# Kernel tuning notes

Hardware: AMD Instinct MI355X
Metric: run time of the kernel (lower is better)

The kernel has to match this reference:

```python
import jax, jax.numpy as jnp
import numpy as np
import math

L, H, P = 16384, 128, 256


def setup_inputs() -> dict:
    key = jax.random.key(0)
    k = jax.random.split(key, 6)
    return {
        "input_sequence": jax.random.normal(k[0], (L, H), dtype=jnp.float32),
        "A_diag": jax.random.uniform(k[1], (P,), dtype=jnp.float32),
        "B": (jax.random.uniform(k[2], (P, H, 2), dtype=jnp.float32) * 2.0 - 1.0) / math.sqrt(H),
        "C": (jax.random.uniform(k[3], (H, P, 2), dtype=jnp.float32) * 2.0 - 1.0) / math.sqrt(P),
        "D": jax.random.normal(k[4], (H,), dtype=jnp.float32),
        "steps": jax.random.uniform(k[5], (P,), dtype=jnp.float32),
    }


def _binop(qi, qj):
    # 2x2 block-diagonal matrix product + affine state propagation, per channel.
    iA, iB, iC, iD, ib1, ib2 = qi
    jA, jB, jC, jD, jb1, jb2 = qj
    return (
        jA * iA + jB * iC,
        jA * iB + jB * iD,
        jC * iA + jD * iC,
        jC * iB + jD * iD,
        jA * ib1 + jB * ib2 + jb1,
        jC * ib1 + jD * ib2 + jb2,
    )


def reference(input_sequence, A_diag, B, C, D, steps):
    # LinOSS-IM discretization (implicit)
    A = jax.nn.relu(A_diag)                      # (P,)
    dt = jax.nn.sigmoid(steps)                   # (P,)
    Bc = B[..., 0] + 1j * B[..., 1]              # (P,H) complex64
    Cc = C[..., 0] + 1j * C[..., 1]              # (H,P) complex64

    Bu = input_sequence @ Bc.T                   # (L,P) complex64

    schur = 1.0 / (1.0 + dt ** 2 * A)
    M11 = 1.0 - dt ** 2 * A * schur
    M12 = -dt * A * schur
    M21 = dt * schur
    M22 = schur

    ones = jnp.ones((input_sequence.shape[0], A.shape[0]), dtype=input_sequence.dtype)
    F1 = M11 * Bu * dt                           # (L,P) complex
    F2 = M21 * Bu * dt

    elems = (M11 * ones, M12 * ones, M21 * ones, M22 * ones, F1, F2)
    _, _, _, _, _, x2 = jax.lax.associative_scan(_binop, elems)  # scan over L

    ys = jnp.real(x2 @ Cc.T)                     # (L,H)
    return ys + input_sequence * D
```

## Files before the change

kernel.cpp:

```cpp
#include <hip/hip_runtime.h>
#include <math.h>

#define L 16384
#define H 128
#define P 256
#define CL 32
#define NCH (L/CL)
#define GS 16
#define NG (NCH/GS)
#define FW 8
#define KDIM 512
#define NBU 512
#define NFLAGS (NCH*FW + NG*FW + 1)

typedef __attribute__((ext_vector_type(8))) short short8;
typedef __attribute__((ext_vector_type(4))) float f32x4;

__device__ inline unsigned short f2bf(float f){
  union { float f; unsigned u; } v; v.f = f;
  unsigned u = v.u;
  u += 0x7fffu + ((u >> 16) & 1u);
  return (unsigned short)(u >> 16);
}
__device__ inline float bf2f(unsigned short s){
  union { unsigned u; float f; } v; v.u = ((unsigned)s) << 16;
  return v.f;
}

struct Params { float M11,M12,M21,M22,s1,s2; };

__device__ inline Params get_params(const float* A_diag, const float* steps, int p){
  float A = A_diag[p]; A = A > 0.f ? A : 0.f;
  float dt = 1.f/(1.f + expf(-steps[p]));
  float schur = 1.f/(1.f + dt*dt*A);
  Params q;
  q.M11 = 1.f - dt*dt*A*schur;
  q.M12 = -dt*A*schur;
  q.M21 = dt*schur;
  q.M22 = schur;
  q.s1 = q.M11*dt;
  q.s2 = q.M21*dt;
  return q;
}

__device__ inline unsigned long long aload(const unsigned long long* p){
  return __hip_atomic_load((unsigned long long*)p, __ATOMIC_RELAXED,
                           __HIP_MEMORY_SCOPE_AGENT);
}
__device__ inline void apub(unsigned long long* p, unsigned long long v){
  (void)__hip_atomic_exchange(p, v, __ATOMIC_RELAXED, __HIP_MEMORY_SCOPE_AGENT);
}
__device__ inline void fpub(unsigned* p){
  (void)__hip_atomic_exchange(p, 1u, __ATOMIC_RELAXED, __HIP_MEMORY_SCOPE_AGENT);
}
__device__ inline void wait_flag(unsigned* f){
  while (__hip_atomic_load(f, __ATOMIC_RELAXED, __HIP_MEMORY_SCOPE_AGENT) == 0u)
    __builtin_amdgcn_s_sleep(1);
}

__global__ __launch_bounds__(512) void prep_w(const float* __restrict__ B,
                                              const float* __restrict__ Cw,
                                              unsigned short* __restrict__ BWswz,
                                              unsigned short* __restrict__ Bswz,
                                              unsigned* __restrict__ flags){
  int gidx = blockIdx.x*512 + threadIdx.x;
  if (gidx < NFLAGS) flags[gidx] = 0u;
  if (gidx < H*NBU){
    int k = gidx >> 9, n = gidx & 511;
    int p = n & 255, c2 = n >> 8;
    float v = B[((size_t)p*H + k)*2 + c2];
    BWswz[((size_t)(k>>3)*NBU + n)*8 + (k&7)] = f2bf(v);
  } else {
    int g2 = gidx - H*NBU;
    int k = g2 >> 7, n = g2 & 127;
    float v = (k < P) ? Cw[((size_t)n*P + k)*2]
                      : -Cw[((size_t)n*P + (k-P))*2 + 1];
    Bswz[((size_t)(k>>3)*H + n)*8 + (k&7)] = f2bf(v);
  }
}

__global__ __launch_bounds__(512, 2) void linoss_fused(
    const float* __restrict__ in,
    const float* __restrict__ A_diag,
    const float* __restrict__ steps,
    const float* __restrict__ Dv,
    const unsigned short* __restrict__ BWswz,
    const unsigned short* __restrict__ Bswz,
    unsigned long long* __restrict__ finals,
    unsigned long long* __restrict__ gfin,
    unsigned* __restrict__ flag1,
    unsigned* __restrict__ flag2,
    unsigned* __restrict__ counter,
    float* __restrict__ out)
{
  __shared__ unsigned short sX[CL][NBU+8];
  __shared__ int s_cid;
  const int tid = threadIdx.x;
  if (tid == 0)
    s_cid = (int)__hip_atomic_fetch_add(counter, 1u, __ATOMIC_RELAXED,
                                        __HIP_MEMORY_SCOPE_AGENT);
  __syncthreads();
  const int c = s_cid;

  {
    int lane = tid & 63, w = tid >> 6;
    int ml = lane & 15, quad = lane >> 4;
    int mt = w & 1, ng = w >> 1;
    int lm0 = mt*16;
    const float* aptr = in + (size_t)(c*CL + lm0 + ml)*H + quad*8;
    float4 fa[8];
    #pragma unroll
    for (int ks=0; ks<4; ks++){
      fa[2*ks]   = *(const float4*)(aptr + ks*32);
      fa[2*ks+1] = *(const float4*)(aptr + ks*32 + 4);
    }
    short8 av[4];
    #pragma unroll
    for (int ks=0; ks<4; ks++){
      union { short8 s; unsigned short u[8]; } o;
      o.u[0]=f2bf(fa[2*ks].x); o.u[1]=f2bf(fa[2*ks].y);
      o.u[2]=f2bf(fa[2*ks].z); o.u[3]=f2bf(fa[2*ks].w);
      o.u[4]=f2bf(fa[2*ks+1].x); o.u[5]=f2bf(fa[2*ks+1].y);
      o.u[6]=f2bf(fa[2*ks+1].z); o.u[7]=f2bf(fa[2*ks+1].w);
      av[ks] = o.s;
    }
    f32x4 acc[8];
    #pragma unroll
    for (int t=0;t<8;t++) acc[t] = (f32x4){0.f,0.f,0.f,0.f};
    #pragma unroll
    for (int ks=0; ks<4; ks++){
      short8 bv[8];
      #pragma unroll
      for (int t=0;t<8;t++)
        bv[t] = *(const short8*)(BWswz + ((size_t)(ks*4+quad)*NBU + (ng*8+t)*16 + ml)*8);
      #pragma unroll
      for (int t=0;t<8;t++)
        acc[t] = __builtin_amdgcn_mfma_f32_16x16x32_bf16(av[ks], bv[t], acc[t], 0, 0, 0);
    }
    #pragma unroll
    for (int t=0;t<8;t++){
      int n = (ng*8+t)*16 + ml;
      #pragma unroll
      for (int r=0;r<4;r++)
        sX[lm0 + quad*4 + r][n] = f2bf(acc[t][r]);
    }
  }
  __syncthreads();

  const int p = tid & 255, part = tid >> 8;
  Params q = get_params(A_diag, steps, p);
  float Ta=q.M11, Tb=q.M12, Tc=q.M21, Td=q.M22;
  #pragma unroll
  for (int s=0;s<5;s++){
    float na=Ta*Ta+Tb*Tc, nb=Ta*Tb+Tb*Td, nc=Tc*Ta+Td*Tc, nd=Tc*Tb+Td*Td;
    Ta=na;Tb=nb;Tc=nc;Td=nd;
  }
  float fx1=0.f, fx2=0.f;
  {
    float u[CL];
    #pragma unroll
    for (int i=0;i<CL;i++) u[i] = bf2f(sX[i][part*256 + p]);
    #pragma unroll
    for (int i=0;i<CL;i++){
      float n1 = q.M11*fx1 + q.M12*fx2 + q.s1*u[i];
      float n2 = q.M21*fx1 + q.M22*fx2 + q.s2*u[i];
      fx1 = n1; fx2 = n2;
    }
  }
  {
    union { unsigned long long u; float2 f; } w; w.f = make_float2(fx1,fx2);
    apub(&finals[(size_t)(part*NCH + c)*P + p], w.u);
  }
  asm volatile("s_waitcnt vmcnt(0)" ::: "memory");
  if ((tid & 63) == 0) fpub(&flag1[c*FW + (tid >> 6)]);

  const int g = c >> 4, iw = c & (GS-1);
  const unsigned long long* Fp = finals + (size_t)part*NCH*P + (size_t)g*GS*P + p;

  float sa=1.f, sb=0.f, sc=0.f, sd=1.f;
  {
    float wa=Ta, wb=Tb, wc=Tc, wd=Td;
    #pragma unroll
    for (int bit=0; bit<4; bit++){
      if ((iw>>bit)&1){
        float na = wa*sa + wb*sc, nb = wa*sb + wb*sd;
        float nc = wc*sa + wd*sc, nd = wc*sb + wd*sd;
        sa=na; sb=nb; sc=nc; sd=nd;
      }
      float qa = wa*wa + wb*wc, qb = wa*wb + wb*wd;
      float qc = wc*wa + wd*wc, qd = wc*wb + wd*wd;
      wa=qa; wb=qb; wc=qc; wd=qd;
    }
  }
  float ga=Ta, gb=Tb, gc=Tc, gd=Td;
  #pragma unroll
  for (int s=0;s<4;s++){
    float na=ga*ga+gb*gc, nb=ga*gb+gb*gd, nc=gc*ga+gd*gc, nd=gc*gb+gd*gd;
    ga=na;gb=nb;gc=nc;gd=nd;
  }

  float z1=0.f, z2v=0.f;
  {
    if (tid < iw*FW) wait_flag(&flag1[(g*GS + (tid>>3))*FW + (tid&7)]);
    __syncthreads();
    unsigned long long v[GS-1];
    #pragma unroll
    for (int j=0;j<GS-1;j++)
      if (j < iw) v[j] = aload(Fp + (size_t)j*P);
    #pragma unroll
    for (int j=0;j<GS-1;j++){
      if (j < iw){
        union { unsigned long long u; float2 f; } w; w.u = v[j];
        float n1 = Ta*z1 + Tb*z2v + w.f.x;
        float n2 = Tc*z1 + Td*z2v + w.f.y;
        z1=n1; z2v=n2;
      }
    }
  }

  if (iw == GS-1){
    float t1 = Ta*z1 + Tb*z2v + fx1;
    float t2 = Tc*z1 + Td*z2v + fx2;
    union { unsigned long long u; float2 f; } w; w.f = make_float2(t1,t2);
    apub(&gfin[(size_t)(part*NG + g)*P + p], w.u);
    asm volatile("s_waitcnt vmcnt(0)" ::: "memory");
    if ((tid & 63) == 0) fpub(&flag2[g*FW + (tid >> 6)]);
  }

  if (tid < g*FW) wait_flag(&flag2[tid]);
  __syncthreads();

  {
    float y1=0.f, y2=0.f;
    {
      const unsigned long long* Gp = gfin + (size_t)part*NG*P + p;
      #pragma unroll
      for (int half=0; half<2; half++){
        unsigned long long v[16];
        #pragma unroll
        for (int j=0;j<16;j++){
          int jj = half*16+j;
          if (jj < g) v[j] = aload(Gp + (size_t)jj*P);
        }
        #pragma unroll
        for (int j=0;j<16;j++){
          int jj = half*16+j;
          if (jj < g){
            union { unsigned long long u; float2 f; } w; w.u = v[j];
            float n1 = ga*y1 + gb*y2 + w.f.x;
            float n2 = gc*y1 + gd*y2 + w.f.y;
            y1=n1; y2=n2;
          }
        }
      }
    }
    float x1 = sa*y1 + sb*y2 + z1;
    float x2 = sc*y1 + sd*y2 + z2v;
    float u[CL];
    #pragma unroll
    for (int i=0;i<CL;i++) u[i] = bf2f(sX[i][part*256 + p]);
    unsigned short hw[CL];
    #pragma unroll
    for (int i=0;i<CL;i++){
      float n1 = q.M11*x1 + q.M12*x2 + q.s1*u[i];
      float n2 = q.M21*x1 + q.M22*x2 + q.s2*u[i];
      x1 = n1; x2 = n2;
      hw[i] = f2bf(x2);
    }
    #pragma unroll
    for (int i=0;i<CL;i++) sX[i][part*256 + p] = hw[i];
  }
  __syncthreads();

  {
    int lane = tid & 63, w = tid >> 6;
    int ml = lane & 15, quad = lane >> 4;
    int mt = w & 1;
    int ntb = (w >> 1) * 2;
    f32x4 acc[2];
    acc[0] = (f32x4){0.f,0.f,0.f,0.f};
    acc[1] = (f32x4){0.f,0.f,0.f,0.f};
    for (int ks=0; ks<KDIM/32; ks++){
      short8 av = *(const short8*)&sX[mt*16 + ml][ks*32 + quad*8];
      short8 bv0 = *(const short8*)(Bswz + ((size_t)(ks*4+quad)*H + (ntb+0)*16 + ml)*8);
      short8 bv1 = *(const short8*)(Bswz + ((size_t)(ks*4+quad)*H + (ntb+1)*16 + ml)*8);
      acc[0] = __builtin_amdgcn_mfma_f32_16x16x32_bf16(av, bv0, acc[0], 0, 0, 0);
      acc[1] = __builtin_amdgcn_mfma_f32_16x16x32_bf16(av, bv1, acc[1], 0, 0, 0);
    }
    #pragma unroll
    for (int j=0;j<2;j++){
      int h = (ntb+j)*16 + ml;
      float dv = Dv[h];
      #pragma unroll
      for (int r=0;r<4;r++){
        int l = c*CL + mt*16 + quad*4 + r;
        out[(size_t)l*H + h] = acc[j][r] + in[(size_t)l*H + h]*dv;
      }
    }
  }
}

extern "C" void kernel_launch(void* const* d_in, const int* in_sizes, int n_in,
                              void* d_out, int out_size, void* d_ws, size_t ws_size,
                              hipStream_t stream) {
  const float* in     = (const float*)d_in[0];
  const float* A_diag = (const float*)d_in[1];
  const float* B      = (const float*)d_in[2];
  const float* Cw     = (const float*)d_in[3];
  const float* Dv     = (const float*)d_in[4];
  const float* steps  = (const float*)d_in[5];
  float* out = (float*)d_out;

  unsigned short* BWswz = (unsigned short*)d_ws;
  unsigned short* Bswz  = BWswz + (size_t)H*NBU;
  unsigned long long* finals = (unsigned long long*)(Bswz + (size_t)KDIM*H);
  unsigned long long* gfin   = finals + (size_t)2*NCH*P;
  unsigned* flags = (unsigned*)(gfin + (size_t)2*NG*P);
  unsigned* flag1 = flags;
  unsigned* flag2 = flags + NCH*FW;
  unsigned* counter = flags + NCH*FW + NG*FW;

  prep_w<<<256, 512, 0, stream>>>(B, Cw, BWswz, Bswz, flags);
  linoss_fused<<<NCH, 512, 0, stream>>>(in, A_diag, steps, Dv, BWswz, Bswz,
                                        finals, gfin, flag1, flag2, counter, out);
}
```

Baseline: 104.6 us.

## Double block size to 1024 threads and split MFMA work across more waves

Result: slower. 115.4 us (+10.3%).

```diff
diff --git a/kernel.cpp b/kernel.cpp
--- a/kernel.cpp
+++ b/kernel.cpp
@@ -79,7 +79,7 @@
   }
 }
 
-__global__ __launch_bounds__(512, 2) void linoss_fused(
+__global__ __launch_bounds__(1024, 4) void linoss_fused(
     const float* __restrict__ in,
     const float* __restrict__ A_diag,
     const float* __restrict__ steps,
@@ -108,38 +108,32 @@
     int mt = w & 1, ng = w >> 1;
     int lm0 = mt*16;
     const float* aptr = in + (size_t)(c*CL + lm0 + ml)*H + quad*8;
-    float4 fa[8];
+    short8 av[4];
     #pragma unroll
     for (int ks=0; ks<4; ks++){
-      fa[2*ks]   = *(const float4*)(aptr + ks*32);
-      fa[2*ks+1] = *(const float4*)(aptr + ks*32 + 4);
-    }
-    short8 av[4];
+      float4 f0 = *(const float4*)(aptr + ks*32);
+      float4 f1 = *(const float4*)(aptr + ks*32 + 4);
+      union { short8 s; unsigned short u[8]; } o;
+      o.u[0]=f2bf(f0.x); o.u[1]=f2bf(f0.y); o.u[2]=f2bf(f0.z); o.u[3]=f2bf(f0.w);
+      o.u[4]=f2bf(f1.x); o.u[5]=f2bf(f1.y); o.u[6]=f2bf(f1.z); o.u[7]=f2bf(f1.w);
+      av[ks] = o.s;
+    }
+    f32x4 acc[4];
+    #pragma unroll
+    for (int t=0;t<4;t++) acc[t] = (f32x4){0.f,0.f,0.f,0.f};
     #pragma unroll
     for (int ks=0; ks<4; ks++){
-      union { short8 s; unsigned short u[8]; } o;
-      o.u[0]=f2bf(fa[2*ks].x); o.u[1]=f2bf(fa[2*ks].y);
-      o.u[2]=f2bf(fa[2*ks].z); o.u[3]=f2bf(fa[2*ks].w);
-      o.u[4]=f2bf(fa[2*ks+1].x); o.u[5]=f2bf(fa[2*ks+1].y);
-      o.u[6]=f2bf(fa[2*ks+1].z); o.u[7]=f2bf(fa[2*ks+1].w);
-      av[ks] = o.s;
-    }
-    f32x4 acc[8];
-    #pragma unroll
-    for (int t=0;t<8;t++) acc[t] = (f32x4){0.f,0.f,0.f,0.f};
-    #pragma unroll
-    for (int ks=0; ks<4; ks++){
-      short8 bv[8];
-      #pragma unroll
-      for (int t=0;t<8;t++)
-        bv[t] = *(const short8*)(BWswz + ((size_t)(ks*4+quad)*NBU + (ng*8+t)*16 + ml)*8);
-      #pragma unroll
-      for (int t=0;t<8;t++)
+      short8 bv[4];
+      #pragma unroll
+      for (int t=0;t<4;t++)
+        bv[t] = *(const short8*)(BWswz + ((size_t)(ks*4+quad)*NBU + (ng*4+t)*16 + ml)*8);
+      #pragma unroll
+      for (int t=0;t<4;t++)
         acc[t] = __builtin_amdgcn_mfma_f32_16x16x32_bf16(av[ks], bv[t], acc[t], 0, 0, 0);
     }
     #pragma unroll
-    for (int t=0;t<8;t++){
-      int n = (ng*8+t)*16 + ml;
+    for (int t=0;t<4;t++){
+      int n = (ng*4+t)*16 + ml;
       #pragma unroll
       for (int r=0;r<4;r++)
         sX[lm0 + quad*4 + r][n] = f2bf(acc[t][r]);
@@ -147,7 +141,8 @@
   }
   __syncthreads();
 
-  const int p = tid & 255, part = tid >> 8;
+  const int p = tid & 255, part = (tid >> 8) & 1;
+  const bool scanner = (tid < 512);
   Params q = get_params(A_diag, steps, p);
   float Ta=q.M11, Tb=q.M12, Tc=q.M21, Td=q.M22;
   #pragma unroll
@@ -156,23 +151,24 @@
     Ta=na;Tb=nb;Tc=nc;Td=nd;
   }
   float fx1=0.f, fx2=0.f;
-  {
-    float u[CL];
-    #pragma unroll
-    for (int i=0;i<CL;i++) u[i] = bf2f(sX[i][part*256 + p]);
-    #pragma unroll
-    for (int i=0;i<CL;i++){
-      float n1 = q.M11*fx1 + q.M12*fx2 + q.s1*u[i];
-      float n2 = q.M21*fx1 + q.M22*fx2 + q.s2*u[i];
-      fx1 = n1; fx2 = n2;
-    }
-  }
-  {
+  if (scanner){
+    #pragma unroll
+    for (int t0=0; t0<CL; t0+=8){
+      float u[8];
+      #pragma unroll
+      for (int j=0;j<8;j++) u[j] = bf2f(sX[t0+j][part*256 + p]);
+      #pragma unroll
+      for (int j=0;j<8;j++){
+        float n1 = q.M11*fx1 + q.M12*fx2 + q.s1*u[j];
+        float n2 = q.M21*fx1 + q.M22*fx2 + q.s2*u[j];
+        fx1 = n1; fx2 = n2;
+      }
+    }
     union { unsigned long long u; float2 f; } w; w.f = make_float2(fx1,fx2);
     apub(&finals[(size_t)(part*NCH + c)*P + p], w.u);
   }
   asm volatile("s_waitcnt vmcnt(0)" ::: "memory");
-  if ((tid & 63) == 0) fpub(&flag1[c*FW + (tid >> 6)]);
+  if (scanner && (tid & 63) == 0) fpub(&flag1[c*FW + (tid >> 6)]);
 
   const int g = c >> 4, iw = c & (GS-1);
   const unsigned long long* Fp = finals + (size_t)part*NCH*P + (size_t)g*GS*P + p;
@@ -199,53 +195,53 @@
     ga=na;gb=nb;gc=nc;gd=nd;
   }
 
+  if (tid < iw*FW) wait_flag(&flag1[(g*GS + (tid>>3))*FW + (tid&7)]);
+  __syncthreads();
   float z1=0.f, z2v=0.f;
-  {
-    if (tid < iw*FW) wait_flag(&flag1[(g*GS + (tid>>3))*FW + (tid&7)]);
-    __syncthreads();
-    unsigned long long v[GS-1];
-    #pragma unroll
-    for (int j=0;j<GS-1;j++)
-      if (j < iw) v[j] = aload(Fp + (size_t)j*P);
-    #pragma unroll
-    for (int j=0;j<GS-1;j++){
-      if (j < iw){
-        union { unsigned long long u; float2 f; } w; w.u = v[j];
-        float n1 = Ta*z1 + Tb*z2v + w.f.x;
-        float n2 = Tc*z1 + Td*z2v + w.f.y;
-        z1=n1; z2v=n2;
+  if (scanner){
+    for (int t0=0; t0<iw; t0+=8){
+      unsigned long long v[8];
+      #pragma unroll
+      for (int j=0;j<8;j++)
+        if (t0+j < iw) v[j] = aload(Fp + (size_t)(t0+j)*P);
+      #pragma unroll
+      for (int j=0;j<8;j++){
+        if (t0+j < iw){
+          union { unsigned long long u; float2 f; } w; w.u = v[j];
+          float n1 = Ta*z1 + Tb*z2v + w.f.x;
+          float n2 = Tc*z1 + Td*z2v + w.f.y;
+          z1=n1; z2v=n2;
+        }
       }
     }
   }
 
   if (iw == GS-1){
-    float t1 = Ta*z1 + Tb*z2v + fx1;
-    float t2 = Tc*z1 + Td*z2v + fx2;
-    union { unsigned long long u; float2 f; } w; w.f = make_float2(t1,t2);
-    apub(&gfin[(size_t)(part*NG + g)*P + p], w.u);
+    if (scanner){
+      float t1 = Ta*z1 + Tb*z2v + fx1;
+      float t2 = Tc*z1 + Td*z2v + fx2;
+      union { unsigned long long u; float2 f; } w; w.f = make_float2(t1,t2);
+      apub(&gfin[(size_t)(part*NG + g)*P + p], w.u);
+    }
     asm volatile("s_waitcnt vmcnt(0)" ::: "memory");
-    if ((tid & 63) == 0) fpub(&flag2[g*FW + (tid >> 6)]);
+    if (scanner && (tid & 63) == 0) fpub(&flag2[g*FW + (tid >> 6)]);
   }
 
   if (tid < g*FW) wait_flag(&flag2[tid]);
   __syncthreads();
 
-  {
+  if (scanner){
     float y1=0.f, y2=0.f;
     {
       const unsigned long long* Gp = gfin + (size_t)part*NG*P + p;
-      #pragma unroll
-      for (int half=0; half<2; half++){
-        unsigned long long v[16];
+      for (int t0=0; t0<g; t0+=8){
+        unsigned long long v[8];
         #pragma unroll
-        for (int j=0;j<16;j++){
-          int jj = half*16+j;
-          if (jj < g) v[j] = aload(Gp + (size_t)jj*P);
-        }
+        for (int j=0;j<8;j++)
+          if (t0+j < g) v[j] = aload(Gp + (size_t)(t0+j)*P);
         #pragma unroll
-        for (int j=0;j<16;j++){
-          int jj = half*16+j;
-          if (jj < g){
+        for (int j=0;j<8;j++){
+          if (t0+j < g){
             union { unsigned long long u; float2 f; } w; w.u = v[j];
             float n1 = ga*y1 + gb*y2 + w.f.x;
             float n2 = gc*y1 + gd*y2 + w.f.y;
@@ -256,46 +252,41 @@
     }
     float x1 = sa*y1 + sb*y2 + z1;
     float x2 = sc*y1 + sd*y2 + z2v;
-    float u[CL];
-    #pragma unroll
-    for (int i=0;i<CL;i++) u[i] = bf2f(sX[i][part*256 + p]);
-    unsigned short hw[CL];
-    #pragma unroll
-    for (int i=0;i<CL;i++){
-      float n1 = q.M11*x1 + q.M12*x2 + q.s1*u[i];
-      float n2 = q.M21*x1 + q.M22*x2 + q.s2*u[i];
-      x1 = n1; x2 = n2;
-      hw[i] = f2bf(x2);
-    }
-    #pragma unroll
-    for (int i=0;i<CL;i++) sX[i][part*256 + p] = hw[i];
+    #pragma unroll
+    for (int t0=0; t0<CL; t0+=8){
+      float u[8];
+      #pragma unroll
+      for (int j=0;j<8;j++) u[j] = bf2f(sX[t0+j][part*256 + p]);
+      unsigned short hw[8];
+      #pragma unroll
+      for (int j=0;j<8;j++){
+        float n1 = q.M11*x1 + q.M12*x2 + q.s1*u[j];
+        float n2 = q.M21*x1 + q.M22*x2 + q.s2*u[j];
+        x1 = n1; x2 = n2;
+        hw[j] = f2bf(x2);
+      }
+      #pragma unroll
+      for (int j=0;j<8;j++) sX[t0+j][part*256 + p] = hw[j];
+    }
   }
   __syncthreads();
 
   {
     int lane = tid & 63, w = tid >> 6;
     int ml = lane & 15, quad = lane >> 4;
-    int mt = w & 1;
-    int ntb = (w >> 1) * 2;
-    f32x4 acc[2];
-    acc[0] = (f32x4){0.f,0.f,0.f,0.f};
-    acc[1] = (f32x4){0.f,0.f,0.f,0.f};
+    int mt = w & 1, nt = w >> 1;
+    f32x4 acc = (f32x4){0.f,0.f,0.f,0.f};
     for (int ks=0; ks<KDIM/32; ks++){
       short8 av = *(const short8*)&sX[mt*16 + ml][ks*32 + quad*8];
-      short8 bv0 = *(const short8*)(Bswz + ((size_t)(ks*4+quad)*H + (ntb+0)*16 + ml)*8);
-      short8 bv1 = *(const short8*)(Bswz + ((size_t)(ks*4+quad)*H + (ntb+1)*16 + ml)*8);
-      acc[0] = __builtin_amdgcn_mfma_f32_16x16x32_bf16(av, bv0, acc[0], 0, 0, 0);
-      acc[1] = __builtin_amdgcn_mfma_f32_16x16x32_bf16(av, bv1, acc[1], 0, 0, 0);
-    }
-    #pragma unroll
-    for (int j=0;j<2;j++){
-      int h = (ntb+j)*16 + ml;
-      float dv = Dv[h];
-      #pragma unroll
-      for (int r=0;r<4;r++){
-        int l = c*CL + mt*16 + quad*4 + r;
-        out[(size_t)l*H + h] = acc[j][r] + in[(size_t)l*H + h]*dv;
-      }
+      short8 bv = *(const short8*)(Bswz + ((size_t)(ks*4+quad)*H + nt*16 + ml)*8);
+      acc = __builtin_amdgcn_mfma_f32_16x16x32_bf16(av, bv, acc, 0, 0, 0);
+    }
+    int h = nt*16 + ml;
+    float dv = Dv[h];
+    #pragma unroll
+    for (int r=0;r<4;r++){
+      int l = c*CL + mt*16 + quad*4 + r;
+      out[(size_t)l*H + h] = acc[r] + in[(size_t)l*H + h]*dv;
     }
   }
 }
@@ -321,6 +312,6 @@
   unsigned* counter = flags + NCH*FW + NG*FW;
 
   prep_w<<<256, 512, 0, stream>>>(B, Cw, BWswz, Bswz, flags);
-  linoss_fused<<<NCH, 512, 0, stream>>>(in, A_diag, steps, Dv, BWswz, Bswz,
-                                        finals, gfin, flag1, flag2, counter, out);
-}
+  linoss_fused<<<NCH, 1024, 0, stream>>>(in, A_diag, steps, Dv, BWswz, Bswz,
+                                         finals, gfin, flag1, flag2, counter, out);
+}
```
